# Kernel tuning notes

Hardware: AMD Instinct MI355X
Metric: run time of the kernel (lower is better)

## Reference

```python
import jax, jax.numpy as jnp
import numpy as np

B, T, H, IN, OUT, FUT = 256, 512, 512, 1, 1, 16


def setup_inputs() -> dict:
    key = jax.random.key(0)
    ks = jax.random.split(key, 11)
    bound = 1.0 / np.sqrt(H)  # torch LSTMCell/Linear default init
    u = lambda kk, sh: jax.random.uniform(kk, sh, jnp.float32, -bound, bound)
    fbias = lambda b: b.at[H:2 * H].set(1.0)  # forget-gate bias filled with 1.0 per __init__
    return {
        "x": jax.random.normal(ks[0], (B, T), jnp.float32),
        "Wih0": u(ks[1], (4 * H, IN)),
        "Whh0": u(ks[2], (4 * H, H)),
        "bih0": fbias(u(ks[3], (4 * H,))),
        "bhh0": fbias(u(ks[4], (4 * H,))),
        "Wih1": u(ks[5], (4 * H, H)),
        "Whh1": u(ks[6], (4 * H, H)),
        "bih1": fbias(u(ks[7], (4 * H,))),
        "bhh1": fbias(u(ks[8], (4 * H,))),
        "Wlin": u(ks[9], (OUT, H)),
        "blin": u(ks[10], (OUT,)),
        "future": FUT,
    }


def _cell(xv, h, c, Wih, Whh, bih, bhh):
    # torch.nn.LSTMCell: gates ordered (i, f, g, o)
    gates = xv @ Wih.T + h @ Whh.T + bih + bhh
    i, f, g, o = jnp.split(gates, 4, axis=-1)
    c = jax.nn.sigmoid(f) * c + jax.nn.sigmoid(i) * jnp.tanh(g)
    h = jax.nn.sigmoid(o) * jnp.tanh(c)
    return h, c


def reference(x, Wih0, Whh0, bih0, bhh0, Wih1, Whh1, bih1, bhh1, Wlin, blin, future):
    params = ((Wih0, Whh0, bih0, bhh0), (Wih1, Whh1, bih1, bhh1))
    Bsz, hid = x.shape[0], Whh0.shape[1]
    h0 = tuple(jnp.zeros((Bsz, hid), x.dtype) for _ in params)
    c0 = tuple(jnp.zeros((Bsz, hid), x.dtype) for _ in params)

    def layer_stack(inp, hs, cs):
        new_h, new_c = [], []
        for j, (Wih, Whh, bih, bhh) in enumerate(params):
            h, c = _cell(inp, hs[j], cs[j], Wih, Whh, bih, bhh)
            new_h.append(h)
            new_c.append(c)
            inp = h
        return tuple(new_h), tuple(new_c), inp

    def cond_step(carry, xt):  # xt: [B, 1]
        hs, cs = carry
        hs, cs, top = layer_stack(xt, hs, cs)
        out = top @ Wlin.T + blin  # [B, 1]
        return (hs, cs), out

    xs = jnp.swapaxes(x, 0, 1)[:, :, None]  # [T, B, 1]
    (hs, cs), outs = jax.lax.scan(cond_step, (h0, c0), xs)
    last = outs[-1]

    def fut_step(carry, _):
        hs, cs, out = carry
        hs, cs, top = layer_stack(out, hs, cs)
        out = top @ Wlin.T + blin
        return (hs, cs, out), out

    _, fut_outs = jax.lax.scan(fut_step, (hs, cs, last), None, length=future)

    all_outs = jnp.concatenate([outs, fut_outs], axis=0)  # [T+future, B, 1]
    return jnp.swapaxes(all_outs, 0, 1)[:, :, 0]  # [B, T+future]
```

## Files before the change

### kernel.cpp

```cpp
#include <hip/hip_runtime.h>
#include <hip/hip_bf16.h>
#include <math.h>

#define HID    512
#define BATCH  256
#define TLEN   512
#define FUT    16
#define NSTEP  (TLEN + FUT)
#define NGRP   16
#define WPG    16
#define BPG    16
#define UPW    32
#define NR     128

#define OFF_W0   0u
#define OFF_W1   2097152u
#define OFF_CA   6291456u
#define OFF_XF   7340032u
#define OFF_WI   7357440u
#define OFF_B0   7365632u
#define OFF_B1   7373824u
#define OFF_BAR  7382016u
#define OFF_XT   7384064u

typedef __bf16 bf16x8 __attribute__((ext_vector_type(8)));
typedef float  f32x4  __attribute__((ext_vector_type(4)));

__device__ __forceinline__ float sigf(float v)      { return 1.f / (1.f + __expf(-v)); }
__device__ __forceinline__ float tanh_fast(float v) { return 2.f / (1.f + __expf(-2.f * v)) - 1.f; }

__device__ __forceinline__ void store_short_llc(void* p, unsigned short v) {
    asm volatile("global_store_short %0, %1, off sc0 sc1"
                 :: "v"(p), "v"((unsigned)v) : "memory");
}

__device__ __forceinline__ void gl2lds16_llc(const void* g, void* l) {
    __builtin_amdgcn_global_load_lds(
        (const __attribute__((address_space(1))) void*)g,
        (__attribute__((address_space(3))) void*)l, 16, 0, 17);
}

__device__ __forceinline__ void flag_barrier(unsigned* flags, int m, unsigned phase) {
    __builtin_amdgcn_s_waitcnt(0);
    __syncthreads();
    if (threadIdx.x == 0)
        __hip_atomic_store(&flags[m], phase, __ATOMIC_RELAXED, __HIP_MEMORY_SCOPE_AGENT);
    if (threadIdx.x < 64) {
        const int lane = threadIdx.x;
        for (;;) {
            unsigned f = phase;
            if (lane < WPG)
                f = __hip_atomic_load(&flags[lane], __ATOMIC_RELAXED, __HIP_MEMORY_SCOPE_AGENT);
            if (__ballot(f >= phase) == ~0ull) break;
            __builtin_amdgcn_s_sleep(1);
        }
    }
    __syncthreads();
}

__global__ void lstm_init(char* __restrict__ ws, float* __restrict__ out,
                          const float* __restrict__ blin)
{
    float bl = blin[0];
    int tid = blockIdx.x * blockDim.x + threadIdx.x;
    int stride = gridDim.x * blockDim.x;
    uint4* ca = (uint4*)(ws + OFF_CA);
    for (int i = tid; i < 65536; i += stride) ca[i] = make_uint4(0u, 0u, 0u, 0u);
    float* xf = (float*)(ws + OFF_XF);
    for (int i = tid; i < (FUT + 1) * BATCH; i += stride) xf[i] = bl;
    unsigned* bar = (unsigned*)(ws + OFF_BAR);
    for (int i = tid; i < NGRP * 32; i += stride) bar[i] = 0u;
    for (int i = tid; i < BATCH * NSTEP; i += stride) out[i] = bl;
}

__global__ void lstm_pack(char* __restrict__ ws,
    const float* __restrict__ x,
    const float* __restrict__ Wih0, const float* __restrict__ Whh0,
    const float* __restrict__ bih0, const float* __restrict__ bhh0,
    const float* __restrict__ Wih1, const float* __restrict__ Whh1,
    const float* __restrict__ bih1, const float* __restrict__ bhh1)
{
    int tid = blockIdx.x * blockDim.x + threadIdx.x;
    int stride = gridDim.x * blockDim.x;

    __hip_bfloat16* W0p = (__hip_bfloat16*)(ws + OFF_W0);
    for (int i = tid; i < 16 * 128 * 512; i += stride) {
        int k = i & 511, r = (i >> 9) & 127, m = i >> 16;
        int row = (r >> 5) * HID + m * UPW + (r & 31);
        W0p[i] = __float2bfloat16(Whh0[(size_t)row * HID + k]);
    }
    __hip_bfloat16* W1p = (__hip_bfloat16*)(ws + OFF_W1);
    for (int i = tid; i < 16 * 128 * 1024; i += stride) {
        int k = i & 1023, r = (i >> 10) & 127, m = i >> 17;
        int row = (r >> 5) * HID + m * UPW + (r & 31);
        float v = (k < 512) ? Wih1[(size_t)row * HID + k] : Whh1[(size_t)row * HID + (k - 512)];
        W1p[i] = __float2bfloat16(v);
    }
    float* wi = (float*)(ws + OFF_WI);
    float* b0 = (float*)(ws + OFF_B0);
    float* b1 = (float*)(ws + OFF_B1);
    for (int i = tid; i < 16 * 128; i += stride) {
        int r = i & 127, m = i >> 7;
        int row = (r >> 5) * HID + m * UPW + (r & 31);
        wi[i] = Wih0[row];
        b0[i] = bih0[row] + bhh0[row];
        b1[i] = bih1[row] + bhh1[row];
    }
    float* xT = (float*)(ws + OFF_XT);
    for (int i = tid; i < TLEN * BATCH; i += stride) {
        int t = i >> 8, b = i & 255;
        xT[i] = x[(size_t)b * TLEN + t];
    }
}

__global__ __launch_bounds__(512, 2) void lstm_persist(
    const float* __restrict__ wlin,
    float* __restrict__ out, char* __restrict__ ws)
{
    const int tid  = threadIdx.x;
    const int lane = tid & 63;
    const int wave = tid >> 6;
    const int g    = blockIdx.x & 15;
    const int m    = blockIdx.x >> 4;
    const int bbase = g * BPG;

    __shared__ __attribute__((aligned(16))) __hip_bfloat16 As[16 * 1024];
    __shared__ float gatesS[16][136];
    char* AsB = (char*)As;

    {
        int* az = (int*)As;
        for (int i = tid; i < (16 * 1024 * 2) / 4; i += 512) az[i] = 0;
    }

    const float* wis = (const float*)(ws + OFF_WI) + m * NR;
    const float* b0s = (const float*)(ws + OFF_B0) + m * NR;
    const float* b1s = (const float*)(ws + OFF_B1) + m * NR;
    char* CAg = ws + OFF_CA + (size_t)g * 65536;
    float* xfeed = (float*)(ws + OFF_XF);
    const float* xT = (const float*)(ws + OFF_XT);
    unsigned* flags = (unsigned*)(ws + OFF_BAR) + g * 32;

    const int fl = lane & 15;
    const int fq = lane >> 4;
    const int w  = wave;
    const int us  = tid & 31;
    const int b0r = tid >> 5;

    const float wl0 = wlin[m * UPW + us];
    float wiR[4], b0R[4], b1R[4];
#pragma unroll
    for (int q = 0; q < 4; ++q) {
        wiR[q] = wis[q * 32 + us];
        b0R[q] = b0s[q * 32 + us];
        b1R[q] = b1s[q * 32 + us];
    }
    float c00 = 0.f, c10 = 0.f;

    const int cgr  = 4 * m + (us >> 3);
    const int pub0 = b0r * 1024 + (((cgr + b0r) & 63) << 4) + (us & 7) * 2;

    const bf16x8* W0row = (const bf16x8*)(ws + OFF_W0 + (size_t)m * NR * 512 * 2)
                          + (size_t)(w * 16 + fl) * 64;
    const bf16x8* W1row = (const bf16x8*)(ws + OFF_W1 + (size_t)m * NR * 1024 * 2)
                          + (size_t)(w * 16 + fl) * 128;
    bf16x8 w0f[16], w1f[32];
#pragma unroll
    for (int ks = 0; ks < 16; ++ks) w0f[ks] = W0row[ks * 4 + fq];
#pragma unroll
    for (int ks = 0; ks < 32; ++ks) w1f[ks] = W1row[ks * 4 + fq];

    __syncthreads();

    const bf16x8* Asv = (const bf16x8*)As;

    unsigned phase = 0;
    for (int t = 0; t < NSTEP; ++t) {
        const int p = t & 1;
        char* CAp = CAg + p * 32768;
        char* CAq = CAg + (1 - p) * 32768;

        float xv0;
        if (t < TLEN) {
            xv0 = xT[t * BATCH + bbase + b0r];
        } else {
            xv0 = xfeed[(t - TLEN) * BATCH + bbase + b0r];
        }

        f32x4 acc0 = {0.f, 0.f, 0.f, 0.f};
#pragma unroll
        for (int ks = 0; ks < 16; ++ks) {
            int c = ks * 4 + fq;
            bf16x8 a0 = Asv[fl * 128 + ((c + fl) & 63)];
            acc0 = __builtin_amdgcn_mfma_f32_16x16x32_bf16(a0, w0f[ks], acc0, 0, 0, 0);
        }
#pragma unroll
        for (int i = 0; i < 4; ++i)
            gatesS[fq * 4 + i][w * 16 + fl] = acc0[i];
        __syncthreads();

        {
            float gi = gatesS[b0r][us]      + b0R[0] + xv0 * wiR[0];
            float gf = gatesS[b0r][32 + us] + b0R[1] + xv0 * wiR[1];
            float gg = gatesS[b0r][64 + us] + b0R[2] + xv0 * wiR[2];
            float go = gatesS[b0r][96 + us] + b0R[3] + xv0 * wiR[3];
            c00 = sigf(gf) * c00 + sigf(gi) * tanh_fast(gg);
            __hip_bfloat16 h = __float2bfloat16(sigf(go) * tanh_fast(c00));
            store_short_llc(CAp + pub0, *(unsigned short*)&h);
        }

        ++phase;
        flag_barrier(flags, m, phase);

        {
#pragma unroll
            for (int ci = 0; ci < 2; ++ci) {
                int b = wave * 2 + ci;
                gl2lds16_llc(CAp + b * 1024 + lane * 16,
                             AsB + b * 2048 + lane * 16);
                gl2lds16_llc(CAq + 16384 + b * 1024 + lane * 16,
                             AsB + b * 2048 + 1024 + lane * 16);
            }
            __builtin_amdgcn_s_waitcnt(0);
            __syncthreads();
        }

        acc0 = (f32x4){0.f, 0.f, 0.f, 0.f};
#pragma unroll
        for (int ks = 0; ks < 16; ++ks) {
            int c = ks * 4 + fq;
            bf16x8 a0 = Asv[fl * 128 + ((c + fl) & 63)];
            acc0 = __builtin_amdgcn_mfma_f32_16x16x32_bf16(a0, w1f[ks], acc0, 0, 0, 0);
        }
#pragma unroll
        for (int ks = 16; ks < 32; ++ks) {
            int c = (ks - 16) * 4 + fq;
            bf16x8 a0 = Asv[fl * 128 + 64 + ((c + fl) & 63)];
            acc0 = __builtin_amdgcn_mfma_f32_16x16x32_bf16(a0, w1f[ks], acc0, 0, 0, 0);
        }
#pragma unroll
        for (int i = 0; i < 4; ++i)
            gatesS[fq * 4 + i][w * 16 + fl] = acc0[i];
        __syncthreads();

        {
            float gi = gatesS[b0r][us]      + b1R[0];
            float gf = gatesS[b0r][32 + us] + b1R[1];
            float gg = gatesS[b0r][64 + us] + b1R[2];
            float go = gatesS[b0r][96 + us] + b1R[3];
            c10 = sigf(gf) * c10 + sigf(gi) * tanh_fast(gg);
            float h = sigf(go) * tanh_fast(c10);
            __hip_bfloat16 hb = __float2bfloat16(h);
            store_short_llc(CAp + 16384 + pub0, *(unsigned short*)&hb);
            float po = wl0 * h;
#pragma unroll
            for (int off = 1; off < 32; off <<= 1) po += __shfl_xor(po, off, 64);
            if (us == 0) {
                atomicAdd(&out[(size_t)(bbase + b0r) * NSTEP + t], po);
                if (t >= TLEN - 1)
                    atomicAdd(&xfeed[(t - (TLEN - 1)) * BATCH + bbase + b0r], po);
            }
        }

        if (t >= TLEN - 1) {
            ++phase;
            flag_barrier(flags, m, phase);
        } else {
            __syncthreads();
        }
    }
}

extern "C" void kernel_launch(void* const* d_in, const int* in_sizes, int n_in,
                              void* d_out, int out_size, void* d_ws, size_t ws_size,
                              hipStream_t stream)
{
    const float* x    = (const float*)d_in[0];
    const float* Wih0 = (const float*)d_in[1];
    const float* Whh0 = (const float*)d_in[2];
    const float* bih0 = (const float*)d_in[3];
    const float* bhh0 = (const float*)d_in[4];
    const float* Wih1 = (const float*)d_in[5];
    const float* Whh1 = (const float*)d_in[6];
    const float* bih1 = (const float*)d_in[7];
    const float* bhh1 = (const float*)d_in[8];
    const float* Wlin = (const float*)d_in[9];
    const float* blin = (const float*)d_in[10];
    float* out = (float*)d_out;
    char* ws = (char*)d_ws;

    hipLaunchKernelGGL(lstm_init, dim3(256), dim3(256), 0, stream, ws, out, blin);
    hipLaunchKernelGGL(lstm_pack, dim3(512), dim3(256), 0, stream,
                       ws, x, Wih0, Whh0, bih0, bhh0, Wih1, Whh1, bih1, bhh1);
    hipLaunchKernelGGL(lstm_persist, dim3(256), dim3(512), 0, stream, Wlin, out, ws);
}
```

Baseline: 2.362 ms.

## Compute next-step layer-0 recurrent gates alongside layer-1 MFMA pass

The layer-0 recurrent matmul for step t+1 is moved into the layer-1 MFMA loop of step t. Both use the same LDS tile: layer-0 h from this step and layer-1 h from the previous step. Results go to a separate g0S buffer, which is zeroed at start for step 0, so the next step's layer-0 cell update can begin without its own MFMA pass and __syncthreads. This drops one serial matmul phase and one barrier per step from the critical path. The cost is an extra shared buffer, more live registers, and reliance on the tile still holding the right h0 when it is reused.

Result: slower. 3.676 ms (+55.6%).

```diff
diff --git a/kernel.cpp b/kernel.cpp
--- a/kernel.cpp
+++ b/kernel.cpp
@@ -125,12 +125,15 @@
     const int bbase = g * BPG;
 
     __shared__ __attribute__((aligned(16))) __hip_bfloat16 As[16 * 1024];
-    __shared__ float gatesS[16][136];
+    __shared__ float g0S[16][136];
+    __shared__ float g1S[16][136];
     char* AsB = (char*)As;
 
     {
         int* az = (int*)As;
         for (int i = tid; i < (16 * 1024 * 2) / 4; i += 512) az[i] = 0;
+        float* gz = &g0S[0][0];
+        for (int i = tid; i < 16 * 136; i += 512) gz[i] = 0.f;
     }
 
     const float* wis = (const float*)(ws + OFF_WI) + m * NR;
@@ -187,23 +190,11 @@
             xv0 = xfeed[(t - TLEN) * BATCH + bbase + b0r];
         }
 
-        f32x4 acc0 = {0.f, 0.f, 0.f, 0.f};
-#pragma unroll
-        for (int ks = 0; ks < 16; ++ks) {
-            int c = ks * 4 + fq;
-            bf16x8 a0 = Asv[fl * 128 + ((c + fl) & 63)];
-            acc0 = __builtin_amdgcn_mfma_f32_16x16x32_bf16(a0, w0f[ks], acc0, 0, 0, 0);
-        }
-#pragma unroll
-        for (int i = 0; i < 4; ++i)
-            gatesS[fq * 4 + i][w * 16 + fl] = acc0[i];
-        __syncthreads();
-
-        {
-            float gi = gatesS[b0r][us]      + b0R[0] + xv0 * wiR[0];
-            float gf = gatesS[b0r][32 + us] + b0R[1] + xv0 * wiR[1];
-            float gg = gatesS[b0r][64 + us] + b0R[2] + xv0 * wiR[2];
-            float go = gatesS[b0r][96 + us] + b0R[3] + xv0 * wiR[3];
+        {
+            float gi = g0S[b0r][us]      + b0R[0] + xv0 * wiR[0];
+            float gf = g0S[b0r][32 + us] + b0R[1] + xv0 * wiR[1];
+            float gg = g0S[b0r][64 + us] + b0R[2] + xv0 * wiR[2];
+            float go = g0S[b0r][96 + us] + b0R[3] + xv0 * wiR[3];
             c00 = sigf(gf) * c00 + sigf(gi) * tanh_fast(gg);
             __hip_bfloat16 h = __float2bfloat16(sigf(go) * tanh_fast(c00));
             store_short_llc(CAp + pub0, *(unsigned short*)&h);
@@ -225,29 +216,35 @@
             __syncthreads();
         }
 
-        acc0 = (f32x4){0.f, 0.f, 0.f, 0.f};
-#pragma unroll
-        for (int ks = 0; ks < 16; ++ks) {
-            int c = ks * 4 + fq;
-            bf16x8 a0 = Asv[fl * 128 + ((c + fl) & 63)];
-            acc0 = __builtin_amdgcn_mfma_f32_16x16x32_bf16(a0, w1f[ks], acc0, 0, 0, 0);
-        }
-#pragma unroll
-        for (int ks = 16; ks < 32; ++ks) {
-            int c = (ks - 16) * 4 + fq;
-            bf16x8 a0 = Asv[fl * 128 + 64 + ((c + fl) & 63)];
-            acc0 = __builtin_amdgcn_mfma_f32_16x16x32_bf16(a0, w1f[ks], acc0, 0, 0, 0);
-        }
-#pragma unroll
-        for (int i = 0; i < 4; ++i)
-            gatesS[fq * 4 + i][w * 16 + fl] = acc0[i];
+        {
+            f32x4 aL1 = {0.f, 0.f, 0.f, 0.f};
+            f32x4 aL0 = {0.f, 0.f, 0.f, 0.f};
+#pragma unroll
+            for (int ks = 0; ks < 16; ++ks) {
+                int c = ks * 4 + fq;
+                bf16x8 a0 = Asv[fl * 128 + ((c + fl) & 63)];
+                aL1 = __builtin_amdgcn_mfma_f32_16x16x32_bf16(a0, w1f[ks], aL1, 0, 0, 0);
+                aL0 = __builtin_amdgcn_mfma_f32_16x16x32_bf16(a0, w0f[ks], aL0, 0, 0, 0);
+            }
+#pragma unroll
+            for (int ks = 16; ks < 32; ++ks) {
+                int c = (ks - 16) * 4 + fq;
+                bf16x8 a0 = Asv[fl * 128 + 64 + ((c + fl) & 63)];
+                aL1 = __builtin_amdgcn_mfma_f32_16x16x32_bf16(a0, w1f[ks], aL1, 0, 0, 0);
+            }
+#pragma unroll
+            for (int i = 0; i < 4; ++i) {
+                g1S[fq * 4 + i][w * 16 + fl] = aL1[i];
+                g0S[fq * 4 + i][w * 16 + fl] = aL0[i];
+            }
+        }
         __syncthreads();
 
         {
-            float gi = gatesS[b0r][us]      + b1R[0];
-            float gf = gatesS[b0r][32 + us] + b1R[1];
-            float gg = gatesS[b0r][64 + us] + b1R[2];
-            float go = gatesS[b0r][96 + us] + b1R[3];
+            float gi = g1S[b0r][us]      + b1R[0];
+            float gf = g1S[b0r][32 + us] + b1R[1];
+            float gg = g1S[b0r][64 + us] + b1R[2];
+            float go = g1S[b0r][96 + us] + b1R[3];
             c10 = sigf(gf) * c10 + sigf(gi) * tanh_fast(gg);
             float h = sigf(go) * tanh_fast(c10);
             __hip_bfloat16 hb = __float2bfloat16(h);
@@ -265,8 +262,6 @@
         if (t >= TLEN - 1) {
             ++phase;
             flag_barrier(flags, m, phase);
-        } else {
-            __syncthreads();
         }
     }
 }
```
